# Kernel tuning notes

Hardware: AMD Instinct MI355X
Metric: run time of the kernel (lower is better)

## Reference

```python
import jax, jax.numpy as jnp
import numpy as np

B, C_IN, C_OUT, H, W = 4, 64, 64, 128, 128
N = 9  # 3x3 sampling points


def setup_inputs() -> dict:
    key = jax.random.key(0)
    k1, k2, k3, k4 = jax.random.split(key, 4)
    x = jax.random.normal(k1, (B, C_IN, H, W), jnp.float32)
    alpha = jax.random.normal(k2, (B, 1, H, W), jnp.float32)
    # kaiming_uniform(a=sqrt(5)) on (C_OUT, C_IN, 3, 3): bound = 1/sqrt(fan_in)
    fan_in = C_IN * 9
    bound = 1.0 / np.sqrt(fan_in)
    weight = jax.random.uniform(k3, (C_OUT, C_IN, 3, 3), jnp.float32, -bound, bound)
    bias = jax.random.uniform(k4, (C_OUT,), jnp.float32, -bound, bound)
    return {"x": x, "alpha": alpha, "weight": weight, "bias": bias}


def _forward(x, alpha, weight, bias):
    b, c, h, w = x.shape
    xp = jnp.pad(x, ((0, 0), (0, 0), (1, 1), (1, 1)))  # ZeroPad2d(1)
    hp, wp = h + 2, w + 2
    dt = x.dtype

    # kernel offsets, N index n = kx*3 + ky (kx slow)
    ks = jnp.arange(-1, 2, dtype=dt)
    pnx = jnp.repeat(ks, 3)  # [-1,-1,-1,0,0,0,1,1,1]
    pny = jnp.tile(ks, 3)    # [-1,0,1,-1,0,1,-1,0,1]

    cosA = jnp.cos(alpha)  # (b,1,h,w)
    sinA = jnp.sin(alpha)
    p0x = jnp.arange(1, h + 1, dtype=dt)[:, None]  # (h,1)
    p0y = jnp.arange(1, w + 1, dtype=dt)[None, :]  # (1,w)
    # note: original code multiplies each coord by (cos +/- sin) of alpha
    px = pnx[None, :, None, None] * (cosA + sinA) + p0x[None, None]  # (b,9,h,w)
    py = pny[None, :, None, None] * (cosA - sinA) + p0y[None, None]
    px = jnp.moveaxis(px, 1, -1)  # (b,h,w,9)
    py = jnp.moveaxis(py, 1, -1)

    fx, fy = jnp.floor(px), jnp.floor(py)  # detached in original (floor grad = 0)
    qx0 = jnp.clip(fx, 0, hp - 1)
    qx1 = jnp.clip(fx + 1, 0, hp - 1)
    qy0 = jnp.clip(fy, 0, wp - 1)
    qy1 = jnp.clip(fy + 1, 0, wp - 1)

    g_lt = (1 + (qx0 - px)) * (1 + (qy0 - py))
    g_rb = (1 - (qx1 - px)) * (1 - (qy1 - py))
    g_lb = (1 + (qx0 - px)) * (1 - (qy1 - py))
    g_rt = (1 - (qx1 - px)) * (1 + (qy0 - py))

    xf = xp.reshape(b, c, hp * wp)
    ix0, ix1 = qx0.astype(jnp.int32), qx1.astype(jnp.int32)
    iy0, iy1 = qy0.astype(jnp.int32), qy1.astype(jnp.int32)

    def gather(ix, iy):
        idx = (ix * wp + iy).reshape(b, -1)  # row-major flatten, like torch gather
        v = jax.vmap(lambda xb, ib: xb[:, ib])(xf, idx)  # (b,c,h*w*9)
        return v.reshape(b, c, h, w, N)

    emap = (g_lt[:, None] * gather(ix0, iy0)
            + g_rb[:, None] * gather(ix1, iy1)
            + g_lb[:, None] * gather(ix0, iy1)
            + g_rt[:, None] * gather(ix1, iy0))  # (b,c,h,w,9)

    # _reshape_x_offset: out[b,c, i*3+ky, j*3+kx] = emap[b,c,i,j, kx*3+ky]
    e = emap.reshape(b, c, h, w, 3, 3)              # (...,kx,ky)
    e = e.transpose(0, 1, 2, 5, 3, 4).reshape(b, c, 3 * h, 3 * w)

    # Dconv: central-difference weights, middle row = -(top + bottom)
    o, i = weight.shape[0], weight.shape[1]
    wr = weight.reshape(o, i, 9)
    r0, r2 = wr[:, :, 0:3], wr[:, :, 6:9]
    buf = jnp.concatenate([r0, -r0 - r2, r2], axis=-1).reshape(o, i, 3, 3)

    y = jax.lax.conv_general_dilated(
        e, buf, window_strides=(3, 3), padding='VALID',
        dimension_numbers=('NCHW', 'OIHW', 'NCHW'))
    return y + bias[None, :, None, None]


def reference(x, alpha, weight, bias):
    return _forward(x, alpha, weight, bias)
```

## Files before the change

kernel.cpp:

```cpp
#include <hip/hip_runtime.h>

#define CIN  64
#define COUT 64
#define Hn   128
#define Wn   128
#define HW   (Hn * Wn)
#define KDIM 576
#define WROW 1152
#define EROW 640

#define NRQ 6
#define NCQ 20
#define NCHUNKQ (NRQ * NCQ * 8)
#define TILE_BYTES (NCHUNKQ * 16)

typedef __attribute__((ext_vector_type(8))) short bf16x8;
typedef __attribute__((ext_vector_type(4))) float f32x4;
typedef __attribute__((ext_vector_type(2))) float f32x2;

__device__ __forceinline__ unsigned short f2bf(float f) {
    unsigned u = __float_as_uint(f);
    unsigned r = u + 0x7FFFu + ((u >> 16) & 1u);
    return (unsigned short)(r >> 16);
}
__device__ __forceinline__ unsigned pk2(float a, float b) {
    return (unsigned)f2bf(a) | ((unsigned)f2bf(b) << 16);
}
__device__ __forceinline__ unsigned pk2h(float a, float b) {
    unsigned ua = __float_as_uint(a) + 0x8000u;
    unsigned ub = __float_as_uint(b) + 0x8000u;
    return __builtin_amdgcn_perm(ub, ua, 0x07060302u);
}


__global__ __launch_bounds__(256) void prep_fused(
    const float* __restrict__ x, const float* __restrict__ weight,
    unsigned short* __restrict__ xt, unsigned short* __restrict__ Wtb2)
{
    __shared__ float fbuf[64][65];
    if (blockIdx.x >= 1024) {
        int e = (blockIdx.x - 1024) * 256 + threadIdx.x;
        if (e < COUT * KDIM) {
            int o = e / KDIM, k = e % KDIM;
            int n = k >> 6, c = k & 63;
            int u = n % 3, v = n / 3;
            float w0 = weight[((o * CIN + c) * 3 + 0) * 3 + v];
            float w2 = weight[((o * CIN + c) * 3 + 2) * 3 + v];
            float val = (u == 0) ? w0 : ((u == 1) ? (-w0 - w2) : w2);
            int s = c >> 5;
            int ce = c & 31;
            Wtb2[((n * 2 + s) * 64 + o) * 32 + ce] = f2bf(val);
        }
        return;
    }
    const int blk = blockIdx.x;
    const int b   = blk >> 8;
    const int rem = blk & 255;
    const int h   = rem >> 1;
    const int w0  = (rem & 1) << 6;
    const int t   = threadIdx.x;
    {
        int wq = t & 63, cq = t >> 6;
        const float* xp = x + ((size_t)(b * CIN + cq * 16) * Hn + h) * Wn + w0 + wq;
        #pragma unroll
        for (int r = 0; r < 16; ++r)
            fbuf[wq][cq * 16 + r] = xp[(size_t)r * HW];
    }
    __syncthreads();
    {
        int wq = t >> 2, q = t & 3;
        const float* row = &fbuf[wq][q * 16];
        uint4 d0, d1;
        d0.x = pk2(row[0],  row[1]);  d0.y = pk2(row[2],  row[3]);
        d0.z = pk2(row[4],  row[5]);  d0.w = pk2(row[6],  row[7]);
        d1.x = pk2(row[8],  row[9]);  d1.y = pk2(row[10], row[11]);
        d1.z = pk2(row[12], row[13]); d1.w = pk2(row[14], row[15]);
        unsigned short* op = xt + ((size_t)(b * Hn + h) * Wn + w0 + wq) * 64 + q * 16;
        *reinterpret_cast<uint4*>(op)     = d0;
        *reinterpret_cast<uint4*>(op + 8) = d1;
    }
}

template<int D>
__device__ __forceinline__ void axis_pts(float s, int base1, int org,
                                         int& l0, int& l1, float& w0, float& w1)
{
    if (D) {
        float p  = (float)D * s + (float)base1;
        float f  = floorf(p);
        float q0 = fminf(fmaxf(f,       0.f), 129.f);
        float q1 = fminf(fmaxf(f + 1.f, 0.f), 129.f);
        w0 = 1.f + (q0 - p);  w1 = 1.f - (q1 - p);
        int i0 = (int)q0, i1 = (int)q1;
        if (i0 < 1 || i0 > 128) w0 = 0.f;
        if (i1 < 1 || i1 > 128) w1 = 0.f;
        l0 = min(max(i0 - 1, 0), 127) - org;
        l1 = min(max(i1 - 1, 0), 127) - org;
    } else {
        l0 = base1 - 1 - org;  w0 = 1.f;
        l1 = l0;               w1 = 0.f;
    }
}

__device__ __forceinline__ void mkpt(int lr, int lc, int g16,
                                     unsigned& offL, unsigned& offH) {
    unsigned base = (unsigned)((lr * NCQ + lc) << 7);
    unsigned m    = ((unsigned)lc & 7u) << 4;
    offL = base + (((unsigned)g16) ^ m);
    offH = base + (((unsigned)(64 + g16)) ^ m);
}

template<int DX, int DY>
__device__ __forceinline__ void geoC(float s1, float s2, int ipx, int iorg,
        int jpx, int jorg, int g16, unsigned oL[4], unsigned oH[4], float gw[4])
{
    int r0, r1, c0, c1; float wx0, wx1, wy0, wy1;
    axis_pts<DX>(s1, ipx + 1, iorg, r0, r1, wx0, wx1);
    axis_pts<DY>(s2, jpx + 1, jorg, c0, c1, wy0, wy1);
    mkpt(r0, c0, g16, oL[0], oH[0]);  gw[0] = wx0 * wy0;
    mkpt(r0, c1, g16, oL[1], oH[1]);  gw[1] = wx0 * wy1;
    mkpt(r1, c0, g16, oL[2], oH[2]);  gw[2] = wx1 * wy0;
    mkpt(r1, c1, g16, oL[3], oH[3]);  gw[3] = wx1 * wy1;
}

template<int DX, int DY>
__device__ __forceinline__ void geoE(float s1, float s2, int ipx, int iorg,
        int jpx, int jorg, int g16, unsigned oL[2], unsigned oH[2], float gw[2])
{
    if (DX == 0) {
        int c0, c1; float wy0, wy1;
        axis_pts<DY>(s2, jpx + 1, jorg, c0, c1, wy0, wy1);
        mkpt(ipx - iorg, c0, g16, oL[0], oH[0]);  gw[0] = wy0;
        mkpt(ipx - iorg, c1, g16, oL[1], oH[1]);  gw[1] = wy1;
    } else {
        int r0, r1; float wx0, wx1;
        axis_pts<DX>(s1, ipx + 1, iorg, r0, r1, wx0, wx1);
        mkpt(r0, jpx - jorg, g16, oL[0], oH[0]);  gw[0] = wx0;
        mkpt(r1, jpx - jorg, g16, oL[1], oH[1]);  gw[1] = wx1;
    }
}

__device__ __forceinline__ f32x2 bfpair(unsigned u) {
    f32x2 r;
    r.x = __uint_as_float(u << 16);
    r.y = __uint_as_float(u & 0xFFFF0000u);
    return r;
}

__device__ __forceinline__ void fma16p(uint4 rl, uint4 rh, float gw,
                                       f32x2* v0, f32x2* v1) {
    const unsigned* u0 = reinterpret_cast<const unsigned*>(&rl);
    const unsigned* u1 = reinterpret_cast<const unsigned*>(&rh);
    f32x2 g2; g2.x = gw; g2.y = gw;
    #pragma unroll
    for (int q = 0; q < 4; ++q) {
        v0[q] = __builtin_elementwise_fma(g2, bfpair(u0[q]), v0[q]);
        v1[q] = __builtin_elementwise_fma(g2, bfpair(u1[q]), v1[q]);
    }
}

__device__ __forceinline__ bf16x8 packv2(const f32x2* v) {
    uint4 p;
    p.x = pk2h(v[0].x, v[0].y); p.y = pk2h(v[1].x, v[1].y);
    p.z = pk2h(v[2].x, v[2].y); p.w = pk2h(v[3].x, v[3].y);
    union { uint4 u; bf16x8 b; } cv; cv.u = p;
    return cv.b;
}

__global__ __launch_bounds__(256, 3) void ddconv_ws3(
    const unsigned short* __restrict__ xt, const float* __restrict__ alpha,
    const unsigned short* __restrict__ Wtb2, const float* __restrict__ bias,
    float* __restrict__ out)
{
    __shared__ __align__(16) char smem[40960];

    const int blk  = blockIdx.x;
    const int b    = blk >> 9;
    const int rem  = blk & 511;
    const int i0   = (rem >> 3) << 1;
    const int j0   = (rem & 7) << 4;
    const int t    = threadIdx.x;
    const int lane = t & 63;
    const int w    = t >> 6;
    const int llo  = lane & 15;
    const int g    = lane >> 4;
    const int g16  = g * 16;
    const int iorg = i0 - 2, jorg = j0 - 2;

    const char* xtb = (const char*)xt + (size_t)b * HW * 128;
    const char* wt2 = (const char*)Wtb2;
    const int arow  = llo * 64 + g16;

    char* tile = smem;
    uint4    sv[4];
    unsigned sla[4];
    {
        const char* sgp[4];
        #pragma unroll
        for (int k = 0; k < 4; ++k) {
            int q = t + k * 256;
            if (k == 3) q = min(q, NCHUNKQ - 1);
            int slot = q & 7;
            int rc   = q >> 3;
            int row  = rc / NCQ;
            int col  = rc - row * NCQ;
            int ru   = min(max(iorg + row, 0), 127);
            int cu   = min(max(jorg + col, 0), 127);
            sgp[k] = xtb + (size_t)(((ru << 7) + cu) << 7) + (slot << 4);
            sla[k] = ((unsigned)rc << 7) + (((unsigned)slot << 4) ^ (((unsigned)col & 7u) << 4));
        }
        #pragma unroll
        for (int k = 0; k < 4; ++k)
            sv[k] = *reinterpret_cast<const uint4*>(sgp[k]);
    }
    #pragma unroll
    for (int k = 0; k < 3; ++k)
        *reinterpret_cast<uint4*>(tile + sla[k]) = sv[k];
    if (t < NCHUNKQ - 3 * 256)
        *reinterpret_cast<uint4*>(tile + sla[3]) = sv[3];

    const int nn0 = (w==0)?0:(w==1)?2:(w==2)?6:8;
    const int nn1 = (w==0)?1:(w==1)?3:(w==2)?7:5;
    const int cs  = w >> 1;
    bf16x8 Ata[2][4], Atb[2][4], Ac0, Ac1;
    #pragma unroll
    for (int s = 0; s < 2; ++s)
      #pragma unroll
      for (int ot = 0; ot < 4; ++ot) {
        Ata[s][ot] = *reinterpret_cast<const bf16x8*>(wt2 + (nn0*2+s)*4096 + ot*1024 + arow);
        Atb[s][ot] = *reinterpret_cast<const bf16x8*>(wt2 + (nn1*2+s)*4096 + ot*1024 + arow);
      }
    Ac0 = *reinterpret_cast<const bf16x8*>(wt2 + (8+cs)*4096 + ((w&1)*2  )*1024 + arow);
    Ac1 = *reinterpret_cast<const bf16x8*>(wt2 + (8+cs)*4096 + ((w&1)*2+1)*1024 + arow);

    float* sAB = reinterpret_cast<float*>(smem + TILE_BYTES);
    if (t < 32) {
        float a = alpha[(b * Hn + i0 + (t >> 4)) * Wn + j0 + (t & 15)];
        float sa, ca;
        sincosf(a, &sa, &ca);
        sAB[t]      = ca + sa;
        sAB[32 + t] = ca - sa;
    }

    f32x4 acc[2][4];
    #pragma unroll
    for (int pg = 0; pg < 2; ++pg)
      #pragma unroll
      for (int ot = 0; ot < 4; ++ot) acc[pg][ot] = (f32x4){0.f, 0.f, 0.f, 0.f};

    __syncthreads();

    float S1[2], S2[2];
    #pragma unroll
    for (int pg = 0; pg < 2; ++pg) {
        S1[pg] = sAB[pg * 16 + llo];
        S2[pg] = sAB[32 + pg * 16 + llo];
    }

    #pragma unroll
    for (int pg = 0; pg < 2; ++pg) {
        const int ipx = i0 + pg;
        const int jpx = j0 + llo;

        unsigned AL[4], AH[4], BL[2], BH[2];
        float    AG[4], BG[2];
        if (w == 0) {
            geoC<-1,-1>(S1[pg], S2[pg], ipx, iorg, jpx, jorg, g16, AL, AH, AG);
            geoE<-1, 0>(S1[pg], S2[pg], ipx, iorg, jpx, jorg, g16, BL, BH, BG);
        } else if (w == 1) {
            geoC<-1, 1>(S1[pg], S2[pg], ipx, iorg, jpx, jorg, g16, AL, AH, AG);
            geoE< 0,-1>(S1[pg], S2[pg], ipx, iorg, jpx, jorg, g16, BL, BH, BG);
        } else if (w == 2) {
            geoC< 1,-1>(S1[pg], S2[pg], ipx, iorg, jpx, jorg, g16, AL, AH, AG);
            geoE< 1, 0>(S1[pg], S2[pg], ipx, iorg, jpx, jorg, g16, BL, BH, BG);
        } else {
            geoC< 1, 1>(S1[pg], S2[pg], ipx, iorg, jpx, jorg, g16, AL, AH, AG);
            geoE< 0, 1>(S1[pg], S2[pg], ipx, iorg, jpx, jorg, g16, BL, BH, BG);
        }
        const int lcc  = jpx - jorg;
        unsigned cb    = (unsigned)((((ipx - iorg) * NCQ) + lcc) << 7);
        unsigned cm    = ((unsigned)lcc & 7u) << 4;
        unsigned cAddr = cb + ((cs ? (unsigned)(64 + g16) : (unsigned)g16) ^ cm);

        uint4 La[4], Ha[4];
        #pragma unroll
        for (int p = 0; p < 4; ++p) {
            La[p] = *reinterpret_cast<const uint4*>(tile + AL[p]);
            Ha[p] = *reinterpret_cast<const uint4*>(tile + AH[p]);
        }
        uint4 Lb[2], Hb[2];
        #pragma unroll
        for (int p = 0; p < 2; ++p) {
            Lb[p] = *reinterpret_cast<const uint4*>(tile + BL[p]);
            Hb[p] = *reinterpret_cast<const uint4*>(tile + BH[p]);
        }
        bf16x8 bc = *reinterpret_cast<const bf16x8*>(tile + cAddr);

        f32x2 v0[4], v1[4];
        #pragma unroll
        for (int q = 0; q < 4; ++q) { v0[q] = (f32x2){0.f,0.f}; v1[q] = (f32x2){0.f,0.f}; }
        #pragma unroll
        for (int p = 0; p < 4; ++p) fma16p(La[p], Ha[p], AG[p], v0, v1);
        bf16x8 bA0 = packv2(v0), bA1 = packv2(v1);

        f32x2 u0[4], u1[4];
        #pragma unroll
        for (int q = 0; q < 4; ++q) { u0[q] = (f32x2){0.f,0.f}; u1[q] = (f32x2){0.f,0.f}; }
        #pragma unroll
        for (int p = 0; p < 2; ++p) fma16p(Lb[p], Hb[p], BG[p], u0, u1);
        bf16x8 bB0 = packv2(u0), bB1 = packv2(u1);

        #pragma unroll
        for (int ot = 0; ot < 4; ++ot) {
            acc[pg][ot] = __builtin_amdgcn_mfma_f32_16x16x32_bf16(Ata[0][ot], bA0, acc[pg][ot], 0, 0, 0);
            acc[pg][ot] = __builtin_amdgcn_mfma_f32_16x16x32_bf16(Ata[1][ot], bA1, acc[pg][ot], 0, 0, 0);
            acc[pg][ot] = __builtin_amdgcn_mfma_f32_16x16x32_bf16(Atb[0][ot], bB0, acc[pg][ot], 0, 0, 0);
            acc[pg][ot] = __builtin_amdgcn_mfma_f32_16x16x32_bf16(Atb[1][ot], bB1, acc[pg][ot], 0, 0, 0);
        }
        if (w & 1) {
            acc[pg][2] = __builtin_amdgcn_mfma_f32_16x16x32_bf16(Ac0, bc, acc[pg][2], 0, 0, 0);
            acc[pg][3] = __builtin_amdgcn_mfma_f32_16x16x32_bf16(Ac1, bc, acc[pg][3], 0, 0, 0);
        } else {
            acc[pg][0] = __builtin_amdgcn_mfma_f32_16x16x32_bf16(Ac0, bc, acc[pg][0], 0, 0, 0);
            acc[pg][1] = __builtin_amdgcn_mfma_f32_16x16x32_bf16(Ac1, bc, acc[pg][1], 0, 0, 0);
        }
    }

    __syncthreads();
    #pragma unroll
    for (int pg = 0; pg < 2; ++pg)
      #pragma unroll
      for (int ot = 0; ot < 4; ++ot)
        *reinterpret_cast<f32x4*>(smem + ((pg*256 + w*64 + lane)*80) + ot*16) = acc[pg][ot];
    __syncthreads();
    {
        const int eq = w;
        #pragma unroll
        for (int pg = 0; pg < 2; ++pg) {
            f32x4 s = (f32x4){0.f, 0.f, 0.f, 0.f};
            #pragma unroll
            for (int ww = 0; ww < 4; ++ww)
                s += *reinterpret_cast<const f32x4*>(smem + ((pg*256 + ww*64 + lane)*80) + eq*16);
            float* ob = out + (size_t)b * COUT * HW + (size_t)(i0 + pg) * Wn + j0 + llo;
            #pragma unroll
            for (int r = 0; r < 4; ++r) {
                int o = eq * 16 + g * 4 + r;
                ob[(size_t)o * HW] = s[r] + bias[o];
            }
        }
    }
}


__global__ void prep_weights(const float* __restrict__ weight,
                             unsigned short* __restrict__ Wtb) {
    int e = blockIdx.x * 256 + threadIdx.x;
    if (e >= COUT * KDIM) return;
    int o = e / KDIM, k = e % KDIM;
    int n = k >> 6, c = k & 63;
    int u = n % 3, v = n / 3;
    float w0 = weight[((o * CIN + c) * 3 + 0) * 3 + v];
    float w2 = weight[((o * CIN + c) * 3 + 2) * 3 + v];
    float val = (u == 0) ? w0 : ((u == 1) ? (-w0 - w2) : w2);
    Wtb[o * KDIM + k] = f2bf(val);
}

template<int DX, int DY>
__device__ __forceinline__ void gatherG(const float* __restrict__ xb,
    float s1, float s2, int i, int jj, int klocal,
    char* myrow, unsigned swz, int c0s, int c1s)
{
    int ix0 = 0, ix1 = 0; float wx0 = 1.f, wx1 = 0.f;
    if (DX != 0) {
        float px = (float)DX * s1 + (float)(i + 1);
        float fx = floorf(px);
        float qx0 = fminf(fmaxf(fx, 0.f), 129.f);
        float qx1 = fminf(fmaxf(fx + 1.f, 0.f), 129.f);
        wx0 = 1.f + (qx0 - px); wx1 = 1.f - (qx1 - px);
        ix0 = (int)qx0; ix1 = (int)qx1;
    } else { ix0 = i + 1; }
    int iy0 = 0, iy1 = 0; float wy0 = 1.f, wy1 = 0.f;
    if (DY != 0) {
        float py = (float)DY * s2 + (float)(jj + 1);
        float fy = floorf(py);
        float qy0 = fminf(fmaxf(fy, 0.f), 129.f);
        float qy1 = fminf(fmaxf(fy + 1.f, 0.f), 129.f);
        wy0 = 1.f + (qy0 - py); wy1 = 1.f - (qy1 - py);
        iy0 = (int)qy0; iy1 = (int)qy1;
    } else { iy0 = jj + 1; }

    constexpr int NX = (DX ? 2 : 1), NY = (DY ? 2 : 1), NT = NX * NY;
    unsigned idx[NT]; float g[NT];
    const int   ixs[2] = { ix0, ix1 };  const float wxs[2] = { wx0, wx1 };
    const int   iys[2] = { iy0, iy1 };  const float wys[2] = { wy0, wy1 };
    #pragma unroll
    for (int xi = 0; xi < NX; ++xi)
      #pragma unroll
      for (int yi = 0; yi < NY; ++yi) {
        int ix = ixs[xi], iy = iys[yi];
        bool ok = (ix >= 1) && (ix <= Hn) && (iy >= 1) && (iy <= Wn);
        int cx = min(max(ix, 1), Hn) - 1;
        int cy = min(max(iy, 1), Wn) - 1;
        idx[xi * NY + yi] = (unsigned)(cx * Wn + cy);
        g[xi * NY + yi]   = ok ? wxs[xi] * wys[yi] : 0.f;
      }
    for (int c0 = c0s; c0 < c1s; c0 += 8) {
        float v[8];
        #pragma unroll
        for (int cc = 0; cc < 8; ++cc) {
            unsigned coff = (unsigned)(c0 + cc) * HW;
            float acc2 = 0.f;
            #pragma unroll
            for (int tp = 0; tp < NT; ++tp)
                acc2 = fmaf(g[tp], xb[coff + idx[tp]], acc2);
            v[cc] = acc2;
        }
        uint4 d;
        d.x = pk2(v[0], v[1]); d.y = pk2(v[2], v[3]);
        d.z = pk2(v[4], v[5]); d.w = pk2(v[6], v[7]);
        unsigned addr = (unsigned)(klocal + c0) * 2u;
        *reinterpret_cast<uint4*>(myrow + (addr ^ swz)) = d;
    }
}

template<int KS>
__device__ __forceinline__ void mfma_phase(const char* emap,
    const unsigned short* __restrict__ Wtb,
    int w, int lane, int passbyte, f32x4 acc[4])
{
    const int llo = lane & 15, lhi = lane >> 4;
    const unsigned prow = (unsigned)(w * 16 + llo);
    const unsigned psw  = (prow & 7u) << 4;
    const char* erow = emap + prow * EROW;
    const char* wtb  = (const char*)Wtb + passbyte + lhi * 16;
    #pragma unroll
    for (int s = 0; s < KS; ++s) {
        unsigned kb = (unsigned)(s * 64 + lhi * 16);
        bf16x8 bf = *reinterpret_cast<const bf16x8*>(erow + (kb ^ psw));
        #pragma unroll
        for (int ot = 0; ot < 4; ++ot) {
            const char* ap = wtb + (ot * 16 + llo) * WROW + s * 64;
            bf16x8 af = *reinterpret_cast<const bf16x8*>(ap);
            acc[ot] = __builtin_amdgcn_mfma_f32_16x16x32_bf16(af, bf, acc[ot], 0, 0, 0);
        }
    }
}

__global__ __launch_bounds__(256, 3) void ddconv_mfma(
    const float* __restrict__ x, const float* __restrict__ alpha,
    const unsigned short* __restrict__ Wtb, const float* __restrict__ bias,
    float* __restrict__ out)
{
    __shared__ __align__(16) char emap[64 * EROW];
    const int blk  = blockIdx.x;
    const int b    = blk >> 8;
    const int rem  = blk & 255;
    const int i    = rem >> 1;
    const int j0   = (rem & 1) << 6;
    const int t    = threadIdx.x;
    const int lane = t & 63;
    const int w    = t >> 6;
    const int jj   = j0 + lane;
    const float* xb = x + (size_t)b * CIN * HW;
    float a = alpha[(b * Hn + i) * Wn + jj];
    float sa, ca;
    sincosf(a, &sa, &ca);
    const float s1 = ca + sa, s2 = ca - sa;
    char* myrow = emap + lane * EROW;
    const unsigned swz = (unsigned)((lane & 7) << 4);
    f32x4 acc[4];
    #pragma unroll
    for (int ot = 0; ot < 4; ++ot) acc[ot] = (f32x4){0.f, 0.f, 0.f, 0.f};
    if (w == 0)      { gatherG<-1,-1>(xb, s1, s2, i, jj,   0, myrow, swz,  0, 48); }
    else if (w == 1) { gatherG<-1,-1>(xb, s1, s2, i, jj,   0, myrow, swz, 48, 64);
                       gatherG<-1, 0>(xb, s1, s2, i, jj,  64, myrow, swz,  0, 64); }
    else if (w == 2) { gatherG<-1, 1>(xb, s1, s2, i, jj, 128, myrow, swz,  0, 48); }
    else             { gatherG<-1, 1>(xb, s1, s2, i, jj, 128, myrow, swz, 48, 64);
                       gatherG< 0,-1>(xb, s1, s2, i, jj, 192, myrow, swz,  0, 64); }
    __syncthreads();
    mfma_phase<8>(emap, Wtb, w, lane, 0, acc);
    __syncthreads();
    if (w == 0)      { gatherG< 1,-1>(xb, s1, s2, i, jj, 128, myrow, swz,  0, 56); }
    else if (w == 1) { gatherG< 1,-1>(xb, s1, s2, i, jj, 128, myrow, swz, 56, 64);
                       gatherG< 1, 1>(xb, s1, s2, i, jj, 256, myrow, swz,  0, 48); }
    else if (w == 2) { gatherG< 1, 1>(xb, s1, s2, i, jj, 256, myrow, swz, 48, 64);
                       gatherG< 0, 1>(xb, s1, s2, i, jj,  64, myrow, swz,  0, 64); }
    else             { gatherG< 1, 0>(xb, s1, s2, i, jj, 192, myrow, swz,  0, 64);
                       gatherG< 0, 0>(xb, s1, s2, i, jj,   0, myrow, swz,  0, 64); }
    __syncthreads();
    mfma_phase<10>(emap, Wtb, w, lane, 512, acc);
    const int llo = lane & 15, lhi = lane >> 4;
    float* ob = out + (size_t)b * COUT * HW + (size_t)i * Wn + j0 + w * 16 + llo;
    #pragma unroll
    for (int ot = 0; ot < 4; ++ot)
      #pragma unroll
      for (int r = 0; r < 4; ++r) {
        int o = ot * 16 + lhi * 4 + r;
        ob[(size_t)o * HW] = acc[ot][r] + bias[o];
      }
}


extern "C" void kernel_launch(void* const* d_in, const int* in_sizes, int n_in,
                              void* d_out, int out_size, void* d_ws, size_t ws_size,
                              hipStream_t stream) {
    const float* x      = (const float*)d_in[0];
    const float* alpha  = (const float*)d_in[1];
    const float* weight = (const float*)d_in[2];
    const float* bias   = (const float*)d_in[3];
    float* out = (float*)d_out;

    const size_t WT_BYTES = (size_t)COUT * KDIM * 2;
    const size_t XT_BYTES = (size_t)4 * HW * CIN * 2;

    if (ws_size >= WT_BYTES + XT_BYTES) {
        unsigned short* Wtb2 = (unsigned short*)d_ws;
        unsigned short* xt   = (unsigned short*)((char*)d_ws + WT_BYTES);
        prep_fused<<<1168, 256, 0, stream>>>(x, weight, xt, Wtb2);
        ddconv_ws3<<<4 * (Hn / 2) * (Wn / 16), 256, 0, stream>>>(xt, alpha, Wtb2, bias, out);
    } else {
        unsigned short* Wtb = (unsigned short*)d_ws;
        prep_weights<<<(COUT * KDIM + 255) / 256, 256, 0, stream>>>(weight, Wtb);
        ddconv_mfma<<<4 * Hn * (Wn / 64), 256, 0, stream>>>(x, alpha, Wtb, bias, out);
    }
}
```

Before: 32.41 us.

## Pad LDS pixel stride, use hardware bf16 pack, merge geometry helpers

```diff
diff --git a/kernel.cpp b/kernel.cpp
--- a/kernel.cpp
+++ b/kernel.cpp
@@ -12,7 +12,8 @@
 #define NRQ 6
 #define NCQ 20
 #define NCHUNKQ (NRQ * NCQ * 8)
-#define TILE_BYTES (NCHUNKQ * 16)
+#define PIXB 144
+#define TILE_BYTES (NRQ * NCQ * PIXB)
 
 typedef __attribute__((ext_vector_type(8))) short bf16x8;
 typedef __attribute__((ext_vector_type(4))) float f32x4;
@@ -23,13 +24,10 @@
     unsigned r = u + 0x7FFFu + ((u >> 16) & 1u);
     return (unsigned short)(r >> 16);
 }
-__device__ __forceinline__ unsigned pk2(float a, float b) {
-    return (unsigned)f2bf(a) | ((unsigned)f2bf(b) << 16);
-}
-__device__ __forceinline__ unsigned pk2h(float a, float b) {
-    unsigned ua = __float_as_uint(a) + 0x8000u;
-    unsigned ub = __float_as_uint(b) + 0x8000u;
-    return __builtin_amdgcn_perm(ub, ua, 0x07060302u);
+__device__ __forceinline__ unsigned pk2c(float a, float b) {
+    unsigned r;
+    asm("v_cvt_pk_bf16_f32 %0, %1, %2" : "=v"(r) : "v"(a), "v"(b));
+    return r;
 }
 
 
@@ -71,10 +69,10 @@
         int wq = t >> 2, q = t & 3;
         const float* row = &fbuf[wq][q * 16];
         uint4 d0, d1;
-        d0.x = pk2(row[0],  row[1]);  d0.y = pk2(row[2],  row[3]);
-        d0.z = pk2(row[4],  row[5]);  d0.w = pk2(row[6],  row[7]);
-        d1.x = pk2(row[8],  row[9]);  d1.y = pk2(row[10], row[11]);
-        d1.z = pk2(row[12], row[13]); d1.w = pk2(row[14], row[15]);
+        d0.x = pk2c(row[0],  row[1]);  d0.y = pk2c(row[2],  row[3]);
+        d0.z = pk2c(row[4],  row[5]);  d0.w = pk2c(row[6],  row[7]);
+        d1.x = pk2c(row[8],  row[9]);  d1.y = pk2c(row[10], row[11]);
+        d1.z = pk2c(row[12], row[13]); d1.w = pk2c(row[14], row[15]);
         unsigned short* op = xt + ((size_t)(b * Hn + h) * Wn + w0 + wq) * 64 + q * 16;
         *reinterpret_cast<uint4*>(op)     = d0;
         *reinterpret_cast<uint4*>(op + 8) = d1;
@@ -85,58 +83,48 @@
 __device__ __forceinline__ void axis_pts(float s, int base1, int org,
                                          int& l0, int& l1, float& w0, float& w1)
 {
-    if (D) {
-        float p  = (float)D * s + (float)base1;
-        float f  = floorf(p);
-        float q0 = fminf(fmaxf(f,       0.f), 129.f);
-        float q1 = fminf(fmaxf(f + 1.f, 0.f), 129.f);
-        w0 = 1.f + (q0 - p);  w1 = 1.f - (q1 - p);
-        int i0 = (int)q0, i1 = (int)q1;
-        if (i0 < 1 || i0 > 128) w0 = 0.f;
-        if (i1 < 1 || i1 > 128) w1 = 0.f;
-        l0 = min(max(i0 - 1, 0), 127) - org;
-        l1 = min(max(i1 - 1, 0), 127) - org;
+    float p  = (float)D * s + (float)base1;
+    float f  = floorf(p);
+    float q0 = fminf(fmaxf(f,       0.f), 129.f);
+    float q1 = fminf(fmaxf(f + 1.f, 0.f), 129.f);
+    w0 = 1.f + (q0 - p);  w1 = 1.f - (q1 - p);
+    int i0 = (int)q0, i1 = (int)q1;
+    if (i0 < 1 || i0 > 128) w0 = 0.f;
+    if (i1 < 1 || i1 > 128) w1 = 0.f;
+    l0 = min(max(i0 - 1, 0), 127) - org;
+    l1 = min(max(i1 - 1, 0), 127) - org;
+}
+
+__device__ __forceinline__ unsigned pixb(int lr, int lc, int g16) {
+    return (unsigned)((lr * NCQ + lc) * PIXB + g16);
+}
+
+template<int DXc, int DYc, int EDX, int EDY>
+__device__ __forceinline__ void geoW(float s1, float s2, int ipx, int iorg,
+        int jpx, int jorg, int g16, unsigned A[4], float AG[4],
+        unsigned B[2], float BG[2])
+{
+    int r0, r1, c0, c1; float wx0, wx1, wy0, wy1;
+    axis_pts<DXc>(s1, ipx + 1, iorg, r0, r1, wx0, wx1);
+    axis_pts<DYc>(s2, jpx + 1, jorg, c0, c1, wy0, wy1);
+    A[0] = pixb(r0, c0, g16);  AG[0] = wx0 * wy0;
+    A[1] = pixb(r0, c1, g16);  AG[1] = wx0 * wy1;
+    A[2] = pixb(r1, c0, g16);  AG[2] = wx1 * wy0;
+    A[3] = pixb(r1, c1, g16);  AG[3] = wx1 * wy1;
+    if (EDY == 0) {
+        int lc = jpx - jorg;
+        B[0] = pixb(r0, lc, g16);  BG[0] = wx0;
+        B[1] = pixb(r1, lc, g16);  BG[1] = wx1;
+    } else if (EDY == DYc) {
+        int lr = ipx - iorg;
+        B[0] = pixb(lr, c0, g16);  BG[0] = wy0;
+        B[1] = pixb(lr, c1, g16);  BG[1] = wy1;
     } else {
-        l0 = base1 - 1 - org;  w0 = 1.f;
-        l1 = l0;               w1 = 0.f;
-    }
-}
-
-__device__ __forceinline__ void mkpt(int lr, int lc, int g16,
-                                     unsigned& offL, unsigned& offH) {
-    unsigned base = (unsigned)((lr * NCQ + lc) << 7);
-    unsigned m    = ((unsigned)lc & 7u) << 4;
-    offL = base + (((unsigned)g16) ^ m);
-    offH = base + (((unsigned)(64 + g16)) ^ m);
-}
-
-template<int DX, int DY>
-__device__ __forceinline__ void geoC(float s1, float s2, int ipx, int iorg,
-        int jpx, int jorg, int g16, unsigned oL[4], unsigned oH[4], float gw[4])
-{
-    int r0, r1, c0, c1; float wx0, wx1, wy0, wy1;
-    axis_pts<DX>(s1, ipx + 1, iorg, r0, r1, wx0, wx1);
-    axis_pts<DY>(s2, jpx + 1, jorg, c0, c1, wy0, wy1);
-    mkpt(r0, c0, g16, oL[0], oH[0]);  gw[0] = wx0 * wy0;
-    mkpt(r0, c1, g16, oL[1], oH[1]);  gw[1] = wx0 * wy1;
-    mkpt(r1, c0, g16, oL[2], oH[2]);  gw[2] = wx1 * wy0;
-    mkpt(r1, c1, g16, oL[3], oH[3]);  gw[3] = wx1 * wy1;
-}
-
-template<int DX, int DY>
-__device__ __forceinline__ void geoE(float s1, float s2, int ipx, int iorg,
-        int jpx, int jorg, int g16, unsigned oL[2], unsigned oH[2], float gw[2])
-{
-    if (DX == 0) {
-        int c0, c1; float wy0, wy1;
-        axis_pts<DY>(s2, jpx + 1, jorg, c0, c1, wy0, wy1);
-        mkpt(ipx - iorg, c0, g16, oL[0], oH[0]);  gw[0] = wy0;
-        mkpt(ipx - iorg, c1, g16, oL[1], oH[1]);  gw[1] = wy1;
-    } else {
-        int r0, r1; float wx0, wx1;
-        axis_pts<DX>(s1, ipx + 1, iorg, r0, r1, wx0, wx1);
-        mkpt(r0, jpx - jorg, g16, oL[0], oH[0]);  gw[0] = wx0;
-        mkpt(r1, jpx - jorg, g16, oL[1], oH[1]);  gw[1] = wx1;
+        int e0, e1; float v0, v1;
+        axis_pts<EDY>(s2, jpx + 1, jorg, e0, e1, v0, v1);
+        int lr = ipx - iorg;
+        B[0] = pixb(lr, e0, g16);  BG[0] = v0;
+        B[1] = pixb(lr, e1, g16);  BG[1] = v1;
     }
 }
 
@@ -161,8 +149,8 @@
 
 __device__ __forceinline__ bf16x8 packv2(const f32x2* v) {
     uint4 p;
-    p.x = pk2h(v[0].x, v[0].y); p.y = pk2h(v[1].x, v[1].y);
-    p.z = pk2h(v[2].x, v[2].y); p.w = pk2h(v[3].x, v[3].y);
+    p.x = pk2c(v[0].x, v[0].y); p.y = pk2c(v[1].x, v[1].y);
+    p.z = pk2c(v[2].x, v[2].y); p.w = pk2c(v[3].x, v[3].y);
     union { uint4 u; bf16x8 b; } cv; cv.u = p;
     return cv.b;
 }
@@ -196,18 +184,18 @@
     unsigned sla[4];
     {
         const char* sgp[4];
+        const int slot16 = (t & 7) << 4;
         #pragma unroll
         for (int k = 0; k < 4; ++k) {
             int q = t + k * 256;
             if (k == 3) q = min(q, NCHUNKQ - 1);
-            int slot = q & 7;
             int rc   = q >> 3;
             int row  = rc / NCQ;
             int col  = rc - row * NCQ;
             int ru   = min(max(iorg + row, 0), 127);
             int cu   = min(max(jorg + col, 0), 127);
-            sgp[k] = xtb + (size_t)(((ru << 7) + cu) << 7) + (slot << 4);
-            sla[k] = ((unsigned)rc << 7) + (((unsigned)slot << 4) ^ (((unsigned)col & 7u) << 4));
+            sgp[k] = xtb + (size_t)(((ru << 7) + cu) << 7) + slot16;
+            sla[k] = (unsigned)(rc * PIXB) + slot16;
         }
         #pragma unroll
         for (int k = 0; k < 4; ++k)
@@ -257,44 +245,42 @@
         S2[pg] = sAB[32 + pg * 16 + llo];
     }
 
+    #define LDT(o) (*reinterpret_cast<const uint4*>(tile + (o)))
+
     #pragma unroll
     for (int pg = 0; pg < 2; ++pg) {
         const int ipx = i0 + pg;
         const int jpx = j0 + llo;
 
-        unsigned AL[4], AH[4], BL[2], BH[2];
+        unsigned A[4], B[2];
         float    AG[4], BG[2];
         if (w == 0) {
-            geoC<-1,-1>(S1[pg], S2[pg], ipx, iorg, jpx, jorg, g16, AL, AH, AG);
-            geoE<-1, 0>(S1[pg], S2[pg], ipx, iorg, jpx, jorg, g16, BL, BH, BG);
+            geoW<-1,-1,-1, 0>(S1[pg], S2[pg], ipx, iorg, jpx, jorg, g16, A, AG, B, BG);
         } else if (w == 1) {
-            geoC<-1, 1>(S1[pg], S2[pg], ipx, iorg, jpx, jorg, g16, AL, AH, AG);
-            geoE< 0,-1>(S1[pg], S2[pg], ipx, iorg, jpx, jorg, g16, BL, BH, BG);
+            geoW<-1, 1, 0,-1>(S1[pg], S2[pg], ipx, iorg, jpx, jorg, g16, A, AG, B, BG);
         } else if (w == 2) {
-            geoC< 1,-1>(S1[pg], S2[pg], ipx, iorg, jpx, jorg, g16, AL, AH, AG);
-            geoE< 1, 0>(S1[pg], S2[pg], ipx, iorg, jpx, jorg, g16, BL, BH, BG);
+            geoW< 1,-1, 1, 0>(S1[pg], S2[pg], ipx, iorg, jpx, jorg, g16, A, AG, B, BG);
         } else {
-            geoC< 1, 1>(S1[pg], S2[pg], ipx, iorg, jpx, jorg, g16, AL, AH, AG);
-            geoE< 0, 1>(S1[pg], S2[pg], ipx, iorg, jpx, jorg, g16, BL, BH, BG);
-        }
-        const int lcc  = jpx - jorg;
-        unsigned cb    = (unsigned)((((ipx - iorg) * NCQ) + lcc) << 7);
-        unsigned cm    = ((unsigned)lcc & 7u) << 4;
-        unsigned cAddr = cb + ((cs ? (unsigned)(64 + g16) : (unsigned)g16) ^ cm);
+            geoW< 1, 1, 0, 1>(S1[pg], S2[pg], ipx, iorg, jpx, jorg, g16, A, AG, B, BG);
+        }
+        unsigned cAddr = pixb(pg + 2, llo + 2, g16) + (cs ? 64u : 0u);
 
         uint4 La[4], Ha[4];
         #pragma unroll
         for (int p = 0; p < 4; ++p) {
-            La[p] = *reinterpret_cast<const uint4*>(tile + AL[p]);
-            Ha[p] = *reinterpret_cast<const uint4*>(tile + AH[p]);
+            La[p] = LDT(A[p]);
+            Ha[p] = LDT(A[p] + 64);
         }
         uint4 Lb[2], Hb[2];
         #pragma unroll
         for (int p = 0; p < 2; ++p) {
-            Lb[p] = *reinterpret_cast<const uint4*>(tile + BL[p]);
-            Hb[p] = *reinterpret_cast<const uint4*>(tile + BH[p]);
-        }
-        bf16x8 bc = *reinterpret_cast<const bf16x8*>(tile + cAddr);
+            Lb[p] = LDT(B[p]);
+            Hb[p] = LDT(B[p] + 64);
+        }
+        bf16x8 bc;
+        {
+            union { uint4 u; bf16x8 b; } cv; cv.u = LDT(cAddr); bc = cv.b;
+        }
 
         f32x2 v0[4], v1[4];
         #pragma unroll
@@ -325,6 +311,7 @@
             acc[pg][1] = __builtin_amdgcn_mfma_f32_16x16x32_bf16(Ac1, bc, acc[pg][1], 0, 0, 0);
         }
     }
+    #undef LDT
 
     __syncthreads();
     #pragma unroll
@@ -351,6 +338,10 @@
     }
 }
 
+
+__device__ __forceinline__ unsigned pk2f(float a, float b) {
+    return (unsigned)f2bf(a) | ((unsigned)f2bf(b) << 16);
+}
 
 __global__ void prep_weights(const float* __restrict__ weight,
                              unsigned short* __restrict__ Wtb) {
@@ -416,8 +407,8 @@
             v[cc] = acc2;
         }
         uint4 d;
-        d.x = pk2(v[0], v[1]); d.y = pk2(v[2], v[3]);
-        d.z = pk2(v[4], v[5]); d.w = pk2(v[6], v[7]);
+        d.x = pk2f(v[0], v[1]); d.y = pk2f(v[2], v[3]);
+        d.z = pk2f(v[4], v[5]); d.w = pk2f(v[6], v[7]);
         unsigned addr = (unsigned)(klocal + c0) * 2u;
         *reinterpret_cast<uint4*>(myrow + (addr ^ swz)) = d;
     }
```

Result: no change. 31.93 us (-1.5%).
